# Kernel optimization log

Measured on AMD Instinct MI355X. Metric: run time of the kernel, lower is better.

## Reference

```python
import jax, jax.numpy as jnp
import numpy as np

H = 16      # num_heads
DH = 64     # dim_heads


def rotate_half(x):
    # '... (j d) -> ... j d', j=2; unbind -> (x1, x2); cat(-x2, x1)
    x1, x2 = jnp.split(x, 2, axis=-1)
    return jnp.concatenate([-x2, x1], axis=-1)


def apply_rope(t, freqs):
    # t: [b, h, s, d], freqs: [s, d] (rot_dim == d, so no unrotated tail)
    return t * jnp.cos(freqs) + rotate_half(t) * jnp.sin(freqs)


def setup_inputs() -> dict:
    key = jax.random.key(0)
    k1, k2, k3, k4 = jax.random.split(key, 4)
    B, S, D = 2, 2048, 1024
    x = jax.random.normal(k1, (B, S, D), dtype=jnp.float32)
    w_qkv = jax.random.normal(k2, (D, 3 * D), dtype=jnp.float32) * (D ** -0.5)
    w_out = jax.random.normal(k3, (D, D), dtype=jnp.float32) * (D ** -0.5)
    freqs = jax.random.normal(k4, (S, DH), dtype=jnp.float32)
    return {"x": x, "w_qkv": w_qkv, "w_out": w_out, "freqs": freqs}


def reference(x, w_qkv, w_out, freqs):
    B, S, D = x.shape
    qkv = x @ w_qkv                                   # [B, S, 3D]
    q, k, v = jnp.split(qkv, 3, axis=-1)
    def to_heads(t):
        return t.reshape(B, S, H, DH).transpose(0, 2, 1, 3)  # [B, H, S, DH]
    q, k, v = map(to_heads, (q, k, v))
    # rotary (computed in float32, which is already the working dtype)
    q = apply_rope(q, freqs)
    k = apply_rope(k, freqs)
    # causal SDPA, scale = 1/sqrt(dh)
    scale = DH ** -0.5
    scores = jnp.einsum('bhqd,bhkd->bhqk', q, k) * scale
    causal_mask = jnp.tril(jnp.ones((S, S), dtype=bool))
    scores = jnp.where(causal_mask, scores, jnp.finfo(scores.dtype).min)
    attn = jax.nn.softmax(scores, axis=-1)
    out = jnp.einsum('bhqk,bhkd->bhqd', attn, v)      # [B, H, S, DH]
    out = out.transpose(0, 2, 1, 3).reshape(B, S, D)  # 'b h n d -> b n (h d)'
    return out @ w_out
```

## Files before the change

### kernel.cpp

```cpp
#include <hip/hip_runtime.h>


typedef __bf16 bf16x8 __attribute__((ext_vector_type(8)));
typedef float f32x4 __attribute__((ext_vector_type(4)));

__device__ __forceinline__ unsigned short f2b(float f) {
  unsigned int u = __builtin_bit_cast(unsigned int, f);
  unsigned int lsb = (u >> 16) & 1u;
  u += 0x7fffu + lsb;
  return (unsigned short)(u >> 16);
}
__device__ __forceinline__ float b2f(unsigned short h) {
  unsigned int u = ((unsigned int)h) << 16;
  return __builtin_bit_cast(float, u);
}
__device__ __forceinline__ unsigned int pk2(float a, float b) {
  return (unsigned int)f2b(a) | ((unsigned int)f2b(b) << 16);
}
__device__ __forceinline__ unsigned int cvtpk(float lo, float hi) {
  unsigned int r;
  asm("v_cvt_pk_bf16_f32 %0, %1, %2" : "=v"(r) : "v"(lo), "v"(hi));
  return r;
}
__device__ __forceinline__ void gload16(const void* g, void* l) {
  __builtin_amdgcn_global_load_lds(
      (const __attribute__((address_space(1))) unsigned int*)g,
      (__attribute__((address_space(3))) unsigned int*)l, 16, 0, 0);
}

__global__ __launch_bounds__(256) void prologue_kernel(
    const float* __restrict__ x, unsigned short* __restrict__ xb,
    const float* __restrict__ freqs, float* __restrict__ cosT,
    float* __restrict__ sinT, const float* __restrict__ w_qkv,
    unsigned short* __restrict__ wqT, const float* __restrict__ w_out,
    unsigned short* __restrict__ woT) {
  __shared__ float tile[32][33];
  const int blk = blockIdx.x, tid = threadIdx.x;

  if (blk < 4096) {
    int i = (blk * 256 + tid) * 4;
    float4 v = *(const float4*)&x[i];
    ushort4 o;
    o.x = f2b(v.x); o.y = f2b(v.y); o.z = f2b(v.z); o.w = f2b(v.w);
    *(ushort4*)&xb[i] = o;
    return;
  }
  if (blk < 4608) {
    int i = (blk - 4096) * 256 + tid;
    float f = freqs[i];
    cosT[i] = cosf(f);
    sinT[i] = sinf(f);
    return;
  }
  const float* src;
  unsigned short* dst;
  int K, N, bx, by;
  if (blk < 7680) {
    src = w_qkv; dst = wqT; K = 1024; N = 3072;
    const int t = blk - 4608;
    bx = t % 96; by = t / 96;
  } else {
    src = w_out; dst = woT; K = 1024; N = 1024;
    const int t = blk - 7680;
    bx = t % 32; by = t / 32;
  }
  const int n0 = bx * 32, k0 = by * 32;
  const int c = tid & 31, r4 = tid >> 5;
#pragma unroll
  for (int p = 0; p < 4; ++p) {
    int r = r4 + p * 8;
    tile[r][c] = src[(size_t)(k0 + r) * N + n0 + c];
  }
  __syncthreads();
#pragma unroll
  for (int p = 0; p < 4; ++p) {
    int r = r4 + p * 8;
    dst[(size_t)(n0 + r) * K + k0 + c] = f2b(tile[c][r]);
  }
}

__global__ __launch_bounds__(512, 6) void gemm_fused(
    const unsigned short* __restrict__ A, const unsigned short* __restrict__ BT,
    unsigned short* __restrict__ Qb, unsigned short* __restrict__ Kbp,
    unsigned short* __restrict__ Vtg, const float* __restrict__ cosT,
    const float* __restrict__ sinT) {
  extern __shared__ unsigned short L[];
  const int K = 1024;
  const int tid = threadIdx.x, lane = tid & 63, w = tid >> 6;
  const int wr = w >> 1, wc = w & 1;
  const int fr = lane & 15, oct = lane >> 4;

  const int m0 = blockIdx.y * 128, n0 = blockIdx.x * 128;

  const int scol = ((tid & 3) ^ ((tid >> 3) & 3)) * 8;
  const size_t aR = (size_t)(m0 + (tid >> 2)) * K + scol;
  const size_t bR = (size_t)(n0 + (tid >> 2)) * K + scol;

  f32x4 acc[2][4] = {};
  const int T = K >> 5;

  for (int pt = 0; pt < 2; ++pt) {
    unsigned short* Ln = &L[pt * 8192];
    const size_t gk = (size_t)pt * 32;
    gload16(&A[aR + gk], &Ln[tid * 8]);
    gload16(&BT[bR + gk], &Ln[4096 + tid * 8]);
  }

  int cs = 0;
  for (int t = 0; t < T; ++t) {
    if (t + 2 <= T) {
      asm volatile("s_waitcnt vmcnt(2)" ::: "memory");
    } else {
      asm volatile("s_waitcnt vmcnt(0)" ::: "memory");
    }
    __builtin_amdgcn_sched_barrier(0);
    __builtin_amdgcn_s_barrier();
    __builtin_amdgcn_sched_barrier(0);

    const unsigned short* Lb = &L[cs * 8192];
    const int sslot = (cs == 0) ? 2 : cs - 1;
    unsigned short* Ln = &L[sslot * 8192];
    const size_t gk = (size_t)(t + 2) * 32;
    const bool doStage = (t + 2 < T);

    bf16x8 af[2], bq[4];
#pragma unroll
    for (int i = 0; i < 2; ++i) {
      const int ra = wr * 32 + i * 16 + fr;
      af[i] = __builtin_bit_cast(
          bf16x8, *(const uint4*)&Lb[ra * 32 + ((oct ^ ((ra >> 1) & 3)) * 8)]);
    }
#pragma unroll
    for (int j = 0; j < 4; ++j) {
      const int rb = wc * 64 + j * 16 + fr;
      bq[j] = __builtin_bit_cast(
          bf16x8,
          *(const uint4*)&Lb[4096 + rb * 32 + ((oct ^ ((rb >> 1) & 3)) * 8)]);
    }
    if (doStage) {
      gload16(&A[aR + gk], &Ln[tid * 8]);
      gload16(&BT[bR + gk], &Ln[4096 + tid * 8]);
    }
    __builtin_amdgcn_s_setprio(1);
#pragma unroll
    for (int i = 0; i < 2; ++i)
#pragma unroll
      for (int j = 0; j < 4; ++j)
        acc[i][j] = __builtin_amdgcn_mfma_f32_16x16x32_bf16(af[i], bq[j], acc[i][j], 0, 0, 0);
    __builtin_amdgcn_s_setprio(0);

    cs = (cs == 2) ? 0 : cs + 1;
  }

  const float QSCALE = 0.125f * 1.44269504f;
  const int part = n0 >> 10;
  const int hh = ((n0 & 1023) >> 6) + wc;
  if (part < 2) {
    unsigned short* dst = (part == 0) ? Qb : Kbp;
    const float scale = (part == 0) ? QSCALE : 1.0f;
#pragma unroll
    for (int i = 0; i < 2; ++i)
#pragma unroll
      for (int r = 0; r < 4; ++r) {
        const int m = m0 + wr * 32 + i * 16 + oct * 4 + r;
        const int bb = m >> 11, s = m & 2047;
        const size_t ob = ((size_t)(bb * 16 + hh) * 2048 + s) * 64;
#pragma unroll
        for (int j = 0; j < 2; ++j) {
          const int d = j * 16 + fr;
          const float lo = acc[i][j][r], hi = acc[i][j + 2][r];
          const float cl = cosT[s * 64 + d], sl = sinT[s * 64 + d];
          const float ch = cosT[s * 64 + 32 + d], sh = sinT[s * 64 + 32 + d];
          dst[ob + d] = f2b((lo * cl - hi * sl) * scale);
          dst[ob + 32 + d] = f2b((hi * ch + lo * sh) * scale);
        }
      }
  } else {
    __syncthreads();
    unsigned short* vt = L + ((wr >> 1) * 2 + wc) * 4224;
#pragma unroll
    for (int i = 0; i < 2; ++i)
#pragma unroll
      for (int r = 0; r < 4; ++r) {
        const int s64 = (wr & 1) * 32 + i * 16 + oct * 4 + r;
#pragma unroll
        for (int j = 0; j < 4; ++j) vt[s64 * 66 + j * 16 + fr] = f2b(acc[i][j][r]);
      }
    __syncthreads();
    const int tix2 = tid >> 6, d = tid & 63;
    const int tile = tix2 >> 1, qh = tix2 & 1;
    const unsigned short* tt = L + tile * 4224;
    const int mtile = m0 + (tile >> 1) * 64;
    const int bb = mtile >> 11, sb = (mtile & 2047) >> 6;
    const int hv = ((n0 & 1023) >> 6) + (tile & 1);
    const size_t vb = (((size_t)(bb * 16 + hv) * 32 + sb) * 64 + d) * 64;
#pragma unroll
    for (int q2 = 0; q2 < 2; ++q2) {
      const int qq = qh * 2 + q2;
#pragma unroll
      for (int g = 0; g < 4; ++g) {
        ushort4 u;
        u.x = tt[(qq * 16 + g * 4 + 0) * 66 + d];
        u.y = tt[(qq * 16 + g * 4 + 1) * 66 + d];
        u.z = tt[(qq * 16 + g * 4 + 2) * 66 + d];
        u.w = tt[(qq * 16 + g * 4 + 3) * 66 + d];
        *(ushort4*)&Vtg[vb + (qq >> 1) * 32 + g * 8 + (qq & 1) * 4] = u;
      }
    }
  }
}

__global__ __launch_bounds__(256, 2) void gemm2_ring(const unsigned short* __restrict__ A,
                                                     const unsigned short* __restrict__ BT,
                                                     float* __restrict__ C,
                                                     int M, int N, int K) {
  extern __shared__ unsigned short L[];
  const int tid = threadIdx.x, lane = tid & 63, w = tid >> 6;
  const int wr = w >> 1, wc = w & 1;
  const int fr = lane & 15, oct = lane >> 4;
  const int m0 = blockIdx.y * 128, n0 = blockIdx.x * 64;

  const int sr = tid >> 2;
  const int scol = ((tid & 3) ^ ((tid >> 3) & 3)) * 8;
  const size_t aR0 = (size_t)(m0 + sr) * K + scol;
  const size_t aR1 = (size_t)(m0 + 64 + sr) * K + scol;
  const size_t bR0 = (size_t)(n0 + sr) * K + scol;

  f32x4 acc[4][2] = {};
  const int T = K >> 5;

  for (int pt = 0; pt < 3; ++pt) {
    unsigned short* Ln = &L[pt * 6144];
    const size_t gk = (size_t)pt * 32;
    gload16(&A[aR0 + gk], &Ln[tid * 8]);
    gload16(&A[aR1 + gk], &Ln[2048 + tid * 8]);
    gload16(&BT[bR0 + gk], &Ln[4096 + tid * 8]);
  }

  for (int t = 0; t < T; ++t) {
    if (t + 3 <= T) {
      asm volatile("s_waitcnt vmcnt(6)" ::: "memory");
    } else if (t + 2 == T) {
      asm volatile("s_waitcnt vmcnt(3)" ::: "memory");
    } else {
      asm volatile("s_waitcnt vmcnt(0)" ::: "memory");
    }
    __builtin_amdgcn_sched_barrier(0);
    __builtin_amdgcn_s_barrier();
    __builtin_amdgcn_sched_barrier(0);

    const unsigned short* Lb = &L[(t & 3) * 6144];
    unsigned short* Ln = &L[((t + 3) & 3) * 6144];
    const size_t gk = (size_t)(t + 3) * 32;
    const bool doStage = (t + 3 < T);

    bf16x8 af[4], bq[2];
#pragma unroll
    for (int i = 0; i < 4; ++i) {
      const int ra = wr * 64 + i * 16 + fr;
      af[i] = __builtin_bit_cast(
          bf16x8, *(const uint4*)&Lb[ra * 32 + ((oct ^ ((ra >> 1) & 3)) * 8)]);
    }
#pragma unroll
    for (int j = 0; j < 2; ++j) {
      const int rb = wc * 32 + j * 16 + fr;
      bq[j] = __builtin_bit_cast(
          bf16x8,
          *(const uint4*)&Lb[4096 + rb * 32 + ((oct ^ ((rb >> 1) & 3)) * 8)]);
    }
    if (doStage) {
      gload16(&A[aR0 + gk], &Ln[tid * 8]);
      gload16(&A[aR1 + gk], &Ln[2048 + tid * 8]);
      gload16(&BT[bR0 + gk], &Ln[4096 + tid * 8]);
    }
    __builtin_amdgcn_s_setprio(1);
#pragma unroll
    for (int i = 0; i < 4; ++i)
#pragma unroll
      for (int j = 0; j < 2; ++j)
        acc[i][j] = __builtin_amdgcn_mfma_f32_16x16x32_bf16(af[i], bq[j], acc[i][j], 0, 0, 0);
    __builtin_amdgcn_s_setprio(0);
  }

#pragma unroll
  for (int i = 0; i < 4; ++i)
#pragma unroll
    for (int j = 0; j < 2; ++j)
#pragma unroll
      for (int r = 0; r < 4; ++r)
        C[(size_t)(m0 + wr * 64 + i * 16 + oct * 4 + r) * N + n0 + wc * 32 +
          j * 16 + fr] = acc[i][j][r];
}

__global__ __launch_bounds__(512, 4) void attn_mfma(const unsigned short* __restrict__ Qb,
                                                    const unsigned short* __restrict__ Kb,
                                                    const unsigned short* __restrict__ Vtg,
                                                    unsigned short* __restrict__ attnb) {
  extern __shared__ unsigned short KV[];
  const int bid = blockIdx.x + 16 * (blockIdx.y + 16 * blockIdx.z);
  const int xcd = bid & 7, slot = bid >> 3;
  const int qt0 = slot & 15;
  const int gq = xcd + 8 * (slot >> 4);
  const int h = gq & 15, b = gq >> 4;
  const int qt1 = 31 - qt0;
  const int tid = threadIdx.x, lane = tid & 63, w = tid >> 6;
  const int fr = lane & 15, oct = lane >> 4;
  const int grp = w >> 2, wq = w & 3;
  const int nhA = 16 - qt0, nhB = 15 - qt0;

  const size_t bh = (size_t)(b * 16 + h);
  const unsigned short* Kbase = Kb + bh * 131072;
  const unsigned short* Vbase = Vtg + bh * 131072;

  const int qtP1 = grp ? qt1 : qt0;
  const unsigned short* Qp1 = Qb + (bh * 2048 + qtP1 * 64 + wq * 16 + fr) * 64;
  const bf16x8 qa0 = __builtin_bit_cast(bf16x8, *(const uint4*)(Qp1 + oct * 8));
  const bf16x8 qa1 = __builtin_bit_cast(bf16x8, *(const uint4*)(Qp1 + 32 + oct * 8));
  const unsigned short* Qp2 = Qb + (bh * 2048 + qt1 * 64 + wq * 16 + fr) * 64;
  const bf16x8 qb0 = __builtin_bit_cast(bf16x8, *(const uint4*)(Qp2 + oct * 8));
  const bf16x8 qb1 = __builtin_bit_cast(bf16x8, *(const uint4*)(Qp2 + 32 + oct * 8));

  const int frx = fr & 7;
  const int rc0 = (oct ^ frx) * 8;
  const int rc1 = ((4 + oct) ^ frx) * 8;

  float m_prev = -1e30f;
  f32x4 acc[4] = {};
  f32x4 accl = {};

  uint4 onesu;
  onesu.x = 0x3F803F80u; onesu.y = 0x3F803F80u;
  onesu.z = 0x3F803F80u; onesu.w = 0x3F803F80u;
  const bf16x8 onesf = __builtin_bit_cast(bf16x8, onesu);

  auto tile_step = [&](int buf, bf16x8 q0, bf16x8 q1, bool domask) {
    const unsigned short* Kbuf = &KV[buf * 4096];
    const unsigned short* Vbuf = &KV[(4 + buf) * 4096];
    f32x4 s4[4];
    __builtin_amdgcn_s_setprio(1);
#pragma unroll
    for (int t = 0; t < 4; ++t) {
      bf16x8 kf0 = __builtin_bit_cast(bf16x8, *(const uint4*)&Kbuf[(t * 16 + fr) * 64 + rc0]);
      bf16x8 kf1 = __builtin_bit_cast(bf16x8, *(const uint4*)&Kbuf[(t * 16 + fr) * 64 + rc1]);
      f32x4 s = {};
      s = __builtin_amdgcn_mfma_f32_16x16x32_bf16(kf0, q0, s, 0, 0, 0);
      s = __builtin_amdgcn_mfma_f32_16x16x32_bf16(kf1, q1, s, 0, 0, 0);
      s4[t] = s;
    }
    __builtin_amdgcn_s_setprio(0);
    if (domask) {
#pragma unroll
      for (int t = 0; t < 4; ++t)
#pragma unroll
        for (int r = 0; r < 4; ++r)
          if (t * 16 + oct * 4 + r > wq * 16 + fr) s4[t][r] = -1e30f;
    }

    float pm = -1e30f;
#pragma unroll
    for (int t = 0; t < 4; ++t)
#pragma unroll
      for (int r = 0; r < 4; ++r) pm = fmaxf(pm, s4[t][r]);
    const bool need = __any(pm - m_prev > 11.0f);
    if (need) {
      float pmf = fmaxf(pm, __shfl_xor(pm, 16));
      pmf = fmaxf(pmf, __shfl_xor(pmf, 32));
      float mnew = fmaxf(m_prev, pmf);
      float cf = __builtin_amdgcn_exp2f(m_prev - mnew);
      m_prev = mnew;
      float cfr[4];
#pragma unroll
      for (int r = 0; r < 4; ++r) cfr[r] = __shfl(cf, oct * 4 + r);
#pragma unroll
      for (int t2 = 0; t2 < 4; ++t2)
#pragma unroll
        for (int r = 0; r < 4; ++r) acc[t2][r] *= cfr[r];
#pragma unroll
      for (int r = 0; r < 4; ++r) accl[r] *= cfr[r];
    }
    const float mc = m_prev;
#pragma unroll
    for (int t = 0; t < 4; ++t)
#pragma unroll
      for (int r = 0; r < 4; ++r)
        s4[t][r] = __builtin_amdgcn_exp2f(s4[t][r] - mc);

    uint4 pw0, pw1;
    pw0.x = cvtpk(s4[0][0], s4[0][1]); pw0.y = cvtpk(s4[0][2], s4[0][3]);
    pw0.z = cvtpk(s4[1][0], s4[1][1]); pw0.w = cvtpk(s4[1][2], s4[1][3]);
    pw1.x = cvtpk(s4[2][0], s4[2][1]); pw1.y = cvtpk(s4[2][2], s4[2][3]);
    pw1.z = cvtpk(s4[3][0], s4[3][1]); pw1.w = cvtpk(s4[3][2], s4[3][3]);
    const bf16x8 pa0 = __builtin_bit_cast(bf16x8, pw0);
    const bf16x8 pa1 = __builtin_bit_cast(bf16x8, pw1);

    __builtin_amdgcn_s_setprio(1);
#pragma unroll
    for (int t2 = 0; t2 < 4; ++t2) {
      bf16x8 vf0 = __builtin_bit_cast(bf16x8, *(const uint4*)&Vbuf[(t2 * 16 + fr) * 64 + rc0]);
      bf16x8 vf1 = __builtin_bit_cast(bf16x8, *(const uint4*)&Vbuf[(t2 * 16 + fr) * 64 + rc1]);
      f32x4 a = acc[t2];
      a = __builtin_amdgcn_mfma_f32_16x16x32_bf16(pa0, vf0, a, 0, 0, 0);
      a = __builtin_amdgcn_mfma_f32_16x16x32_bf16(pa1, vf1, a, 0, 0, 0);
      acc[t2] = a;
    }
    {
      f32x4 a = accl;
      a = __builtin_amdgcn_mfma_f32_16x16x32_bf16(pa0, onesf, a, 0, 0, 0);
      a = __builtin_amdgcn_mfma_f32_16x16x32_bf16(pa1, onesf, a, 0, 0, 0);
      accl = a;
    }
    __builtin_amdgcn_s_setprio(0);
  };

  auto write_out = [&](int qtile) {
#pragma unroll
    for (int r = 0; r < 4; ++r) {
      float linv = 1.f / accl[r];
      size_t orow = (size_t)(b * 2048 + qtile * 64 + wq * 16 + oct * 4 + r);
#pragma unroll
      for (int t2 = 0; t2 < 4; ++t2)
        attnb[orow * 1024 + h * 64 + t2 * 16 + fr] = f2b(acc[t2][r] * linv);
    }
  };

  const int srow = tid >> 3, lc1 = tid & 7;
  const int soff = srow * 64 + (lc1 ^ (srow & 7)) * 8;
  const unsigned short* kp1 = Kbase + srow * 64 + lc1 * 8;
  const unsigned short* vp1 = Vbase + srow * 64 + lc1 * 8;
  {
    uint4 kr = *(const uint4*)kp1;
    uint4 vr = *(const uint4*)vp1;
    *(uint4*)&KV[0 * 4096 + soff] = kr;
    *(uint4*)&KV[4 * 4096 + soff] = vr;
  }
  __syncthreads();

  for (int kb = 0; kb <= qt0; ++kb) {
    uint4 kr = *(const uint4*)(kp1 + (size_t)(kb + 1) * 4096);
    uint4 vr = *(const uint4*)(vp1 + (size_t)(kb + 1) * 4096);
    uint4 kr2, vr2;
    const bool extra = (kb == qt0) && (nhB > 0);
    if (extra) {
      kr2 = *(const uint4*)(kp1 + (size_t)17 * 4096);
      vr2 = *(const uint4*)(vp1 + (size_t)17 * 4096);
    }
    tile_step(kb & 1, qa0, qa1, kb == qtP1);
    const int nb = (kb + 1) & 1;
    *(uint4*)&KV[nb * 4096 + soff] = kr;
    *(uint4*)&KV[(4 + nb) * 4096 + soff] = vr;
    if (extra) {
      *(uint4*)&KV[2 * 4096 + soff] = kr2;
      *(uint4*)&KV[6 * 4096 + soff] = vr2;
    }
    __syncthreads();
  }

  if (grp == 0) {
    write_out(qt0);
    m_prev = -1e30f;
    f32x4 zz = {};
    accl = zz;
#pragma unroll
    for (int t2 = 0; t2 < 4; ++t2) acc[t2] = zz;
  }

  const int t2id = tid & 255;
  const int sk2 = t2id >> 2, lq = t2id & 3;
  const int lcA = lq * 2, lcB = lq * 2 + 1;
  const int ofA = sk2 * 64 + (lcA ^ (sk2 & 7)) * 8;
  const int ofB = sk2 * 64 + (lcB ^ (sk2 & 7)) * 8;
  const int sc2 = lq * 16;
  const int cnt = grp ? nhB : nhA;
  for (int i = 0; i < nhA; ++i) {
    const int kbm = grp ? (17 + i) : (qt0 + 1 + i);
    const int buf = grp ? (2 + (i & 1)) : (kbm & 1);
    uint4 k0, k1, v0, v1;
    const bool pf = (i + 1 < cnt);
    if (pf) {
      const unsigned short* ks = Kbase + (size_t)((kbm + 1) * 64 + sk2) * 64 + sc2;
      const unsigned short* vs = Vbase + (size_t)((kbm + 1) * 64 + sk2) * 64 + sc2;
      k0 = *(const uint4*)ks; k1 = *(const uint4*)(ks + 8);
      v0 = *(const uint4*)vs; v1 = *(const uint4*)(vs + 8);
    }
    if (i < cnt) tile_step(buf, qb0, qb1, kbm == qt1);
    if (pf) {
      const int nb = grp ? (2 + ((i + 1) & 1)) : ((kbm + 1) & 1);
      *(uint4*)&KV[nb * 4096 + ofA] = k0;
      *(uint4*)&KV[nb * 4096 + ofB] = k1;
      *(uint4*)&KV[(4 + nb) * 4096 + ofA] = v0;
      *(uint4*)&KV[(4 + nb) * 4096 + ofB] = v1;
    }
    __syncthreads();
  }

  float* MF = (float*)KV;
  if (grp == 1) {
#pragma unroll
    for (int t2 = 0; t2 < 4; ++t2)
#pragma unroll
      for (int r = 0; r < 4; ++r)
        MF[(wq * 16 + oct * 4 + r) * 68 + t2 * 16 + fr] = acc[t2][r];
    if (fr == 0) {
#pragma unroll
      for (int r = 0; r < 4; ++r) MF[4352 + wq * 16 + oct * 4 + r] = accl[r];
    }
    if (oct == 0) MF[4416 + wq * 16 + fr] = m_prev;
  }
  __syncthreads();
  if (grp == 0) {
    float mB = MF[4416 + wq * 16 + fr];
    float mS = fmaxf(m_prev, mB);
    float fA = __builtin_amdgcn_exp2f(m_prev - mS);
    float fB = __builtin_amdgcn_exp2f(mB - mS);
    float fAr[4], fBr[4];
#pragma unroll
    for (int r = 0; r < 4; ++r) {
      fAr[r] = __shfl(fA, oct * 4 + r);
      fBr[r] = __shfl(fB, oct * 4 + r);
    }
#pragma unroll
    for (int r = 0; r < 4; ++r)
      accl[r] = accl[r] * fAr[r] + MF[4352 + wq * 16 + oct * 4 + r] * fBr[r];
#pragma unroll
    for (int t2 = 0; t2 < 4; ++t2)
#pragma unroll
      for (int r = 0; r < 4; ++r)
        acc[t2][r] = acc[t2][r] * fAr[r] +
                     MF[(wq * 16 + oct * 4 + r) * 68 + t2 * 16 + fr] * fBr[r];
    write_out(qt1);
  }
}

extern "C" void kernel_launch(void* const* d_in, const int* in_sizes, int n_in,
                              void* d_out, int out_size, void* d_ws, size_t ws_size,
                              hipStream_t stream) {
  const float* x     = (const float*)d_in[0];
  const float* w_qkv = (const float*)d_in[1];
  const float* w_out = (const float*)d_in[2];
  const float* freqs = (const float*)d_in[3];
  float* out = (float*)d_out;

  char* ws = (char*)d_ws;
  unsigned short* Qb   = (unsigned short*)(ws + 25165824);
  unsigned short* Kb   = (unsigned short*)(ws + 33554432);
  unsigned short* Vtg  = (unsigned short*)(ws + 41943040);
  unsigned short* attnb= (unsigned short*)(ws + 50331648);
  unsigned short* wqT  = (unsigned short*)(ws + 58720256);
  unsigned short* woT  = (unsigned short*)(ws + 65011712);
  unsigned short* xb   = (unsigned short*)(ws + 67108864);
  float* cosT          = (float*)(ws + 75497472);
  float* sinT          = (float*)(ws + 76021760);

  (void)hipFuncSetAttribute((const void*)gemm_fused,
                            hipFuncAttributeMaxDynamicSharedMemorySize, 49152);
  (void)hipFuncSetAttribute((const void*)gemm2_ring,
                            hipFuncAttributeMaxDynamicSharedMemorySize, 49152);
  (void)hipFuncSetAttribute((const void*)attn_mfma,
                            hipFuncAttributeMaxDynamicSharedMemorySize, 65536);

  prologue_kernel<<<8704, 256, 0, stream>>>(x, xb, freqs, cosT, sinT, w_qkv,
                                            wqT, w_out, woT);
  gemm_fused<<<dim3(24, 32), 512, 49152, stream>>>(xb, wqT, Qb, Kb, Vtg, cosT,
                                                   sinT);
  attn_mfma<<<dim3(16, 16, 2), 512, 65536, stream>>>(Qb, Kb, Vtg, attnb);
  gemm2_ring<<<dim3(16, 32), 256, 49152, stream>>>(attnb, woT, out, 4096, 1024, 1024);
}
```

Baseline: 93.18 us.

## Use 256x256 tiles with double-buffered 64-K stages in QKV GEMM

```diff
diff --git a/kernel.cpp b/kernel.cpp
--- a/kernel.cpp
+++ b/kernel.cpp
@@ -79,7 +79,7 @@
   }
 }
 
-__global__ __launch_bounds__(512, 6) void gemm_fused(
+__global__ __launch_bounds__(512, 2) void gemm8(
     const unsigned short* __restrict__ A, const unsigned short* __restrict__ BT,
     unsigned short* __restrict__ Qb, unsigned short* __restrict__ Kbp,
     unsigned short* __restrict__ Vtg, const float* __restrict__ cosT,
@@ -87,82 +87,93 @@
   extern __shared__ unsigned short L[];
   const int K = 1024;
   const int tid = threadIdx.x, lane = tid & 63, w = tid >> 6;
-  const int wr = w >> 1, wc = w & 1;
+  const int wr = w >> 2, wcn = w & 3;
   const int fr = lane & 15, oct = lane >> 4;
 
-  const int m0 = blockIdx.y * 128, n0 = blockIdx.x * 128;
-
+  const int raw = blockIdx.y * 12 + blockIdx.x;
+  const int swz = (raw & 7) * 24 + (raw >> 3);
+  const int m0 = (swz / 12) * 256, n0 = (swz % 12) * 256;
+
+  const int sRow = tid >> 2;
   const int scol = ((tid & 3) ^ ((tid >> 3) & 3)) * 8;
-  const size_t aR = (size_t)(m0 + (tid >> 2)) * K + scol;
-  const size_t bR = (size_t)(n0 + (tid >> 2)) * K + scol;
-
-  f32x4 acc[2][4] = {};
-  const int T = K >> 5;
-
-  for (int pt = 0; pt < 2; ++pt) {
-    unsigned short* Ln = &L[pt * 8192];
-    const size_t gk = (size_t)pt * 32;
-    gload16(&A[aR + gk], &Ln[tid * 8]);
-    gload16(&BT[bR + gk], &Ln[4096 + tid * 8]);
-  }
-
-  int cs = 0;
-  for (int t = 0; t < T; ++t) {
-    if (t + 2 <= T) {
-      asm volatile("s_waitcnt vmcnt(2)" ::: "memory");
-    } else {
-      asm volatile("s_waitcnt vmcnt(0)" ::: "memory");
-    }
-    __builtin_amdgcn_sched_barrier(0);
-    __builtin_amdgcn_s_barrier();
-    __builtin_amdgcn_sched_barrier(0);
-
-    const unsigned short* Lb = &L[cs * 8192];
-    const int sslot = (cs == 0) ? 2 : cs - 1;
-    unsigned short* Ln = &L[sslot * 8192];
-    const size_t gk = (size_t)(t + 2) * 32;
-    const bool doStage = (t + 2 < T);
-
-    bf16x8 af[2], bq[4];
-#pragma unroll
-    for (int i = 0; i < 2; ++i) {
-      const int ra = wr * 32 + i * 16 + fr;
-      af[i] = __builtin_bit_cast(
-          bf16x8, *(const uint4*)&Lb[ra * 32 + ((oct ^ ((ra >> 1) & 3)) * 8)]);
-    }
-#pragma unroll
-    for (int j = 0; j < 4; ++j) {
-      const int rb = wc * 64 + j * 16 + fr;
-      bq[j] = __builtin_bit_cast(
-          bf16x8,
-          *(const uint4*)&Lb[4096 + rb * 32 + ((oct ^ ((rb >> 1) & 3)) * 8)]);
-    }
-    if (doStage) {
-      gload16(&A[aR + gk], &Ln[tid * 8]);
-      gload16(&BT[bR + gk], &Ln[4096 + tid * 8]);
-    }
-    __builtin_amdgcn_s_setprio(1);
-#pragma unroll
-    for (int i = 0; i < 2; ++i)
-#pragma unroll
-      for (int j = 0; j < 4; ++j)
-        acc[i][j] = __builtin_amdgcn_mfma_f32_16x16x32_bf16(af[i], bq[j], acc[i][j], 0, 0, 0);
-    __builtin_amdgcn_s_setprio(0);
-
-    cs = (cs == 2) ? 0 : cs + 1;
+  const int sOff = sRow * 32 + (tid & 3) * 8;
+  const size_t aS0 = (size_t)(m0 + sRow) * K + scol;
+  const size_t aS1 = (size_t)(m0 + 128 + sRow) * K + scol;
+  const size_t bS0 = (size_t)(n0 + sRow) * K + scol;
+  const size_t bS1 = (size_t)(n0 + 128 + sRow) * K + scol;
+
+  const int pcx = (oct ^ ((fr >> 1) & 3)) * 8;
+
+  f32x4 acc[8][4] = {};
+  const int NT = 16;
+
+#pragma unroll
+  for (int kh = 0; kh < 2; ++kh) {
+    const size_t gk = (size_t)kh * 32;
+    gload16(&A[aS0 + gk], &L[kh * 8192 + sOff]);
+    gload16(&A[aS1 + gk], &L[kh * 8192 + 4096 + sOff]);
+    gload16(&BT[bS0 + gk], &L[16384 + kh * 8192 + sOff]);
+    gload16(&BT[bS1 + gk], &L[16384 + kh * 8192 + 4096 + sOff]);
+  }
+
+  for (int t = 0; t < NT; ++t) {
+    const int buf = t & 1, nbuf = buf ^ 1;
+    const bool doStage = (t + 1 < NT);
+#pragma unroll
+    for (int kh = 0; kh < 2; ++kh) {
+      if (t == NT - 1 && kh == 1) {
+        asm volatile("s_waitcnt vmcnt(0)" ::: "memory");
+      } else {
+        asm volatile("s_waitcnt vmcnt(4)" ::: "memory");
+      }
+      __builtin_amdgcn_sched_barrier(0);
+      __builtin_amdgcn_s_barrier();
+      __builtin_amdgcn_sched_barrier(0);
+
+      const unsigned short* Ab = &L[buf * 32768 + kh * 8192];
+      const unsigned short* Bb = &L[buf * 32768 + 16384 + kh * 8192];
+
+      bf16x8 af[8], bq[4];
+#pragma unroll
+      for (int i = 0; i < 8; ++i) {
+        const int row = wr * 128 + i * 16 + fr;
+        af[i] = __builtin_bit_cast(bf16x8, *(const uint4*)&Ab[row * 32 + pcx]);
+      }
+#pragma unroll
+      for (int c = 0; c < 4; ++c) {
+        const int brow = wcn * 64 + c * 16 + fr;
+        bq[c] = __builtin_bit_cast(bf16x8, *(const uint4*)&Bb[brow * 32 + pcx]);
+      }
+      if (doStage) {
+        const size_t gk = (size_t)(t + 1) * 64 + kh * 32;
+        unsigned short* D = &L[nbuf * 32768 + kh * 8192];
+        gload16(&A[aS0 + gk], &D[sOff]);
+        gload16(&A[aS1 + gk], &D[4096 + sOff]);
+        gload16(&BT[bS0 + gk], &D[16384 + sOff]);
+        gload16(&BT[bS1 + gk], &D[16384 + 4096 + sOff]);
+      }
+      __builtin_amdgcn_s_setprio(1);
+#pragma unroll
+      for (int i = 0; i < 8; ++i)
+#pragma unroll
+        for (int c = 0; c < 4; ++c)
+          acc[i][c] = __builtin_amdgcn_mfma_f32_16x16x32_bf16(af[i], bq[c], acc[i][c], 0, 0, 0);
+      __builtin_amdgcn_s_setprio(0);
+    }
   }
 
   const float QSCALE = 0.125f * 1.44269504f;
   const int part = n0 >> 10;
-  const int hh = ((n0 & 1023) >> 6) + wc;
+  const int hbase = (n0 & 1023) >> 6;
   if (part < 2) {
     unsigned short* dst = (part == 0) ? Qb : Kbp;
     const float scale = (part == 0) ? QSCALE : 1.0f;
-#pragma unroll
-    for (int i = 0; i < 2; ++i)
+    const int hh = hbase + wcn;
+#pragma unroll
+    for (int i = 0; i < 8; ++i)
 #pragma unroll
       for (int r = 0; r < 4; ++r) {
-        const int m = m0 + wr * 32 + i * 16 + oct * 4 + r;
+        const int m = m0 + wr * 128 + i * 16 + oct * 4 + r;
         const int bb = m >> 11, s = m & 2047;
         const size_t ob = ((size_t)(bb * 16 + hh) * 2048 + s) * 64;
 #pragma unroll
@@ -176,36 +187,40 @@
         }
       }
   } else {
-    __syncthreads();
-    unsigned short* vt = L + ((wr >> 1) * 2 + wc) * 4224;
-#pragma unroll
-    for (int i = 0; i < 2; ++i)
-#pragma unroll
-      for (int r = 0; r < 4; ++r) {
-        const int s64 = (wr & 1) * 32 + i * 16 + oct * 4 + r;
-#pragma unroll
-        for (int j = 0; j < 4; ++j) vt[s64 * 66 + j * 16 + fr] = f2b(acc[i][j][r]);
+#pragma unroll
+    for (int p = 0; p < 2; ++p) {
+      __syncthreads();
+      if (wr == p) {
+        unsigned short* vt = L + wcn * 8448;
+#pragma unroll
+        for (int i = 0; i < 8; ++i)
+#pragma unroll
+          for (int r = 0; r < 4; ++r) {
+            const int row = i * 16 + oct * 4 + r;
+#pragma unroll
+            for (int j = 0; j < 4; ++j)
+              vt[row * 66 + j * 16 + fr] = f2b(acc[i][j][r]);
+          }
       }
-    __syncthreads();
-    const int tix2 = tid >> 6, d = tid & 63;
-    const int tile = tix2 >> 1, qh = tix2 & 1;
-    const unsigned short* tt = L + tile * 4224;
-    const int mtile = m0 + (tile >> 1) * 64;
-    const int bb = mtile >> 11, sb = (mtile & 2047) >> 6;
-    const int hv = ((n0 & 1023) >> 6) + (tile & 1);
-    const size_t vb = (((size_t)(bb * 16 + hv) * 32 + sb) * 64 + d) * 64;
-#pragma unroll
-    for (int q2 = 0; q2 < 2; ++q2) {
-      const int qq = qh * 2 + q2;
-#pragma unroll
-      for (int g = 0; g < 4; ++g) {
-        ushort4 u;
-        u.x = tt[(qq * 16 + g * 4 + 0) * 66 + d];
-        u.y = tt[(qq * 16 + g * 4 + 1) * 66 + d];
-        u.z = tt[(qq * 16 + g * 4 + 2) * 66 + d];
-        u.w = tt[(qq * 16 + g * 4 + 3) * 66 + d];
-        *(ushort4*)&Vtg[vb + (qq >> 1) * 32 + g * 8 + (qq & 1) * 4] = u;
-      }
+      __syncthreads();
+      const int sidx = tid >> 6, d = tid & 63;
+      const int hd = sidx & 3, mgl = sidx >> 2;
+      const unsigned short* tt = L + hd * 8448 + mgl * 64 * 66;
+      const int mtile = m0 + (p * 2 + mgl) * 64;
+      const int bb = mtile >> 11, sb = (mtile & 2047) >> 6;
+      const int hv = hbase + hd;
+      const size_t vb = (((size_t)(bb * 16 + hv) * 32 + sb) * 64 + d) * 64;
+#pragma unroll
+      for (int qq = 0; qq < 4; ++qq)
+#pragma unroll
+        for (int g = 0; g < 4; ++g) {
+          ushort4 u;
+          u.x = tt[(qq * 16 + g * 4 + 0) * 66 + d];
+          u.y = tt[(qq * 16 + g * 4 + 1) * 66 + d];
+          u.z = tt[(qq * 16 + g * 4 + 2) * 66 + d];
+          u.w = tt[(qq * 16 + g * 4 + 3) * 66 + d];
+          *(ushort4*)&Vtg[vb + (qq >> 1) * 32 + g * 8 + (qq & 1) * 4] = u;
+        }
     }
   }
 }
@@ -551,8 +566,8 @@
   float* cosT          = (float*)(ws + 75497472);
   float* sinT          = (float*)(ws + 76021760);
 
-  (void)hipFuncSetAttribute((const void*)gemm_fused,
-                            hipFuncAttributeMaxDynamicSharedMemorySize, 49152);
+  (void)hipFuncSetAttribute((const void*)gemm8,
+                            hipFuncAttributeMaxDynamicSharedMemorySize, 131072);
   (void)hipFuncSetAttribute((const void*)gemm2_ring,
                             hipFuncAttributeMaxDynamicSharedMemorySize, 49152);
   (void)hipFuncSetAttribute((const void*)attn_mfma,
@@ -560,8 +575,8 @@
 
   prologue_kernel<<<8704, 256, 0, stream>>>(x, xb, freqs, cosT, sinT, w_qkv,
                                             wqT, w_out, woT);
-  gemm_fused<<<dim3(24, 32), 512, 49152, stream>>>(xb, wqT, Qb, Kb, Vtg, cosT,
-                                                   sinT);
+  gemm8<<<dim3(12, 16), 512, 131072, stream>>>(xb, wqT, Qb, Kb, Vtg, cosT,
+                                               sinT);
   attn_mfma<<<dim3(16, 16, 2), 512, 65536, stream>>>(Qb, Kb, Vtg, attnb);
   gemm2_ring<<<dim3(16, 32), 256, 49152, stream>>>(attnb, woT, out, 4096, 1024, 1024);
 }
```

Result: no change. 91.58 us (-1.7%).
